# Kernel tuning notes

Hardware: AMD Instinct MI355X
Metric: run time of the kernel (lower is better)

## Reference

```python
import jax, jax.numpy as jnp
import numpy as np

N, E = 50000, 800000
DIM_IN, DIM_H, DIM_OUT, HEADS = 128, 16, 64, 8
NEG_SLOPE = 0.2  # PyG GATv2Conv default


def setup_inputs() -> dict:
    key = jax.random.key(0)
    ks = jax.random.split(key, 10)
    s = 0.1
    x = jax.random.normal(ks[0], (N, DIM_IN), jnp.float32)
    edge_index = jax.random.randint(ks[1], (2, E), 0, N, dtype=jnp.int32)
    Wl1 = jax.random.normal(ks[2], (DIM_IN, HEADS * DIM_H), jnp.float32) * s
    Wr1 = jax.random.normal(ks[3], (DIM_IN, HEADS * DIM_H), jnp.float32) * s
    att1 = jax.random.normal(ks[4], (HEADS, DIM_H), jnp.float32) * s
    b1 = jnp.zeros((HEADS * DIM_H,), jnp.float32)
    Wl2 = jax.random.normal(ks[5], (HEADS * DIM_H, DIM_OUT), jnp.float32) * s
    Wr2 = jax.random.normal(ks[6], (HEADS * DIM_H, DIM_OUT), jnp.float32) * s
    att2 = jax.random.normal(ks[7], (1, DIM_OUT), jnp.float32) * s
    b2 = jnp.zeros((DIM_OUT,), jnp.float32)
    return dict(x=x, edge_index=edge_index, Wl1=Wl1, Wr1=Wr1, att1=att1, b1=b1,
                Wl2=Wl2, Wr2=Wr2, att2=att2, b2=b2)


def gatv2_conv(x, src, dst, Wl, Wr, att, bias, heads, out_ch):
    # PyG GATv2Conv (share_weights=False, concat=True)
    n = x.shape[0]
    xl = (x @ Wl).reshape(n, heads, out_ch)  # source-side transform
    xr = (x @ Wr).reshape(n, heads, out_ch)  # target-side transform
    e = jax.nn.leaky_relu(xl[src] + xr[dst], NEG_SLOPE)          # [E, H, C]
    logits = jnp.einsum('ehc,hc->eh', e, att)                    # [E, H]
    # segment softmax over incoming edges of each dst node
    m = jax.lax.stop_gradient(jax.ops.segment_max(logits, dst, num_segments=n))
    ex = jnp.exp(logits - m[dst])
    denom = jax.ops.segment_sum(ex, dst, num_segments=n)
    alpha = ex / denom[dst]                                      # [E, H]
    out = jax.ops.segment_sum(xl[src] * alpha[..., None], dst, num_segments=n)
    return out.reshape(n, heads * out_ch) + bias


def reference(x, edge_index, Wl1, Wr1, att1, b1, Wl2, Wr2, att2, b2):
    n = x.shape[0]
    loops = jnp.arange(n, dtype=edge_index.dtype)
    src = jnp.concatenate([edge_index[0], loops])  # add_self_loops=True
    dst = jnp.concatenate([edge_index[1], loops])
    h = gatv2_conv(x, src, dst, Wl1, Wr1, att1, b1, HEADS, DIM_H)
    h = jax.nn.elu(h)
    out = gatv2_conv(h, src, dst, Wl2, Wr2, att2, b2, 1, DIM_OUT)
    return jax.nn.log_softmax(out, axis=1)
```

## Files before the change

kernel.cpp:

```cpp
#include <hip/hip_runtime.h>
#include <cstdint>

#define DIM_IN 128
#define HEADS 8
#define DIM_H 16
#define H1 128
#define DIM_OUT 64
#define NEG 0.2f
#define CAP 6144
#define P1CH 1024

typedef __attribute__((ext_vector_type(8))) short bf16x8;
typedef __attribute__((ext_vector_type(4))) float f32x4;

__device__ __forceinline__ float blo(uint32_t u) { return __uint_as_float(u << 16); }
__device__ __forceinline__ float bhi(uint32_t u) { return __uint_as_float(u & 0xffff0000u); }
__device__ __forceinline__ unsigned short f2b(float f) {
  uint32_t u = __float_as_uint(f);
  u += 0x7fffu + ((u >> 16) & 1u);
  return (unsigned short)(u >> 16);
}

#define KP 0.86561702453337804f
#define KM 0.57707801635558536f

__global__ __launch_bounds__(256) void prep_p1_fused(
    const float* __restrict__ x, unsigned short* __restrict__ xb, int totx,
    const float* __restrict__ W0, const float* __restrict__ W1,
    const float* __restrict__ W2, const float* __restrict__ W3,
    unsigned short* __restrict__ T0, unsigned short* __restrict__ T1,
    unsigned short* __restrict__ T2, unsigned short* __restrict__ T3,
    int xblocks, int p1b,
    const int* __restrict__ ei, int* __restrict__ gcnt,
    uint32_t* __restrict__ gbuf, int E, int nbkt) {
  __shared__ int sh[768];
  int bx = blockIdx.x;
  if (bx < p1b) {
    int* hist = sh;
    int* base = sh + 256;
    int* cur  = sh + 512;
    int tid = threadIdx.x;
    hist[tid] = 0;
    __syncthreads();
    int e0 = bx * P1CH;
    int nE = min(P1CH, E - e0);
    for (int i = tid; i < nE; i += 256)
      atomicAdd(&hist[ei[E + e0 + i] >> 8], 1);
    __syncthreads();
    if (tid < nbkt) {
      int h = hist[tid];
      base[tid] = h ? atomicAdd(&gcnt[tid], h) : 0;
    }
    cur[tid] = 0;
    __syncthreads();
    for (int i = tid; i < nE; i += 256) {
      int d = ei[E + e0 + i];
      int s = ei[e0 + i];
      int b = d >> 8;
      int r = atomicAdd(&cur[b], 1);
      int pos = base[b] + r;
      if (pos < CAP) gbuf[(size_t)b * CAP + pos] = ((uint32_t)d << 16) | (uint32_t)s;
    }
  } else if (bx < p1b + xblocks) {
    int i = ((bx - p1b) * 256 + threadIdx.x) * 8;
    if (i >= totx) return;
    float4 a = *(const float4*)(x + i);
    float4 b = *(const float4*)(x + i + 4);
    ushort4 u0 = {f2b(a.x), f2b(a.y), f2b(a.z), f2b(a.w)};
    ushort4 u1 = {f2b(b.x), f2b(b.y), f2b(b.z), f2b(b.w)};
    *(ushort4*)(xb + i) = u0;
    *(ushort4*)(xb + i + 4) = u1;
  } else {
    int wz = bx - p1b - xblocks;
    int z = wz >> 6;
    const float* W = (z == 0) ? W0 : (z == 1) ? W1 : (z == 2) ? W2 : W3;
    unsigned short* T = (z == 0) ? T0 : (z == 1) ? T1 : (z == 2) ? T2 : T3;
    int M = (z < 2) ? 128 : 64;
    int t = (wz & 63) * 256 + threadIdx.x;
    if (t >= M * 128) return;
    int n = t >> 7, k = t & 127;
    T[t] = f2b(W[k * M + n]);
  }
}

__device__ __forceinline__ int block_excl_scan256(int v, int* tmp) {
  int lane = threadIdx.x & 63, wid = threadIdx.x >> 6;
  int x = v;
#pragma unroll
  for (int o = 1; o < 64; o <<= 1) {
    int y = __shfl_up(x, o, 64);
    if (lane >= o) x += y;
  }
  if (lane == 63) tmp[wid] = x;
  __syncthreads();
  int prefix = 0;
#pragma unroll
  for (int w = 0; w < 4; ++w) if (w < wid) prefix += tmp[w];
  __syncthreads();
  return prefix + x - v;
}

template <int M>
__global__ __launch_bounds__(256) void gemm_mfma(
    const unsigned short* __restrict__ A,
    const unsigned short* __restrict__ Bt0, const unsigned short* __restrict__ Bt1,
    unsigned short* __restrict__ C0, unsigned short* __restrict__ C1, int Nrows,
    int gbx,
    const uint32_t* __restrict__ gbuf, const int* __restrict__ gcnt,
    int* __restrict__ off, int* __restrict__ srcs, int Np, int nbkt) {
  constexpr int K = 128;
  constexpr int LDA = 72;
  constexpr int MT = M / 2;
  constexpr int NT = MT / 16;
  __shared__ __align__(16) short Asm[128 * LDA];
  __shared__ __align__(16) short Bsm[M * LDA];
  if (blockIdx.x >= gbx) {
    if (blockIdx.z != 0) return;
    int* sb   = (int*)Asm;
    int* hist = sb + 256;
    int* cur  = hist + 256;
    int* tmp  = cur + 256;
    int b = blockIdx.x - gbx, tid = threadIdx.x;
    int gv = (tid < nbkt) ? gcnt[tid] : 0;
    int gex = block_excl_scan256(gv, tmp);
    sb[tid] = gex;
    hist[tid] = 0;
    __syncthreads();
    int base = sb[b];
    int cnt = min(gcnt[b], CAP);
    const uint32_t* p = gbuf + (size_t)b * CAP;
    for (int i = tid; i < cnt; i += 256)
      atomicAdd(&hist[(p[i] >> 16) & 255], 1);
    __syncthreads();
    int d = hist[tid];
    int excl = block_excl_scan256(d, tmp);
    int idx = (b << 8) + tid;
    int o = base + excl;
    if (idx <= Np) off[idx] = o;
    cur[tid] = o;
    __syncthreads();
    for (int i = tid; i < cnt; i += 256) {
      uint32_t v = p[i];
      int pos = atomicAdd(&cur[(v >> 16) & 255], 1);
      srcs[pos] = (int)(v & 0xFFFFu);
    }
    return;
  }
  const unsigned short* __restrict__ Bt = blockIdx.z ? Bt1 : Bt0;
  unsigned short* __restrict__ Cb = blockIdx.z ? C1 : C0;
  const int row0 = blockIdx.x * 128;
  const int tid = threadIdx.x;
  const int w = tid >> 6, lane = tid & 63;
  const int l = lane & 15, q = lane >> 4;
  const int wrow = (w >> 1) * 64, wcol = (w & 1) * MT;

  f32x4 zero = {0.f, 0.f, 0.f, 0.f};
  f32x4 acc[4][NT];
#pragma unroll
  for (int ti = 0; ti < 4; ++ti)
#pragma unroll
    for (int tj = 0; tj < NT; ++tj) acc[ti][tj] = zero;

  for (int k0 = 0; k0 < K; k0 += 64) {
    __syncthreads();
    {
      int r = tid >> 1, sg = (tid & 1) * 32;
      int grow = row0 + r;
      const uint4* src = (const uint4*)(A + (size_t)grow * K + k0 + sg);
      uint4 z4 = make_uint4(0, 0, 0, 0);
#pragma unroll
      for (int i = 0; i < 4; ++i) {
        uint4 v = (grow < Nrows) ? src[i] : z4;
        *(uint4*)(Asm + r * LDA + sg + i * 8) = v;
      }
    }
    {
      int r = tid >> 1, sg = (tid & 1) * 32;
      if (r < M) {
        const uint4* src = (const uint4*)(Bt + (size_t)r * K + k0 + sg);
#pragma unroll
        for (int i = 0; i < 4; ++i)
          *(uint4*)(Bsm + r * LDA + sg + i * 8) = src[i];
      }
    }
    __syncthreads();
#pragma unroll
    for (int kk = 0; kk < 64; kk += 32) {
      bf16x8 af[4], bfr[NT];
#pragma unroll
      for (int ti = 0; ti < 4; ++ti)
        af[ti] = *(const bf16x8*)(Asm + (wrow + ti * 16 + l) * LDA + kk + q * 8);
#pragma unroll
      for (int tj = 0; tj < NT; ++tj)
        bfr[tj] = *(const bf16x8*)(Bsm + (wcol + tj * 16 + l) * LDA + kk + q * 8);
#pragma unroll
      for (int ti = 0; ti < 4; ++ti)
#pragma unroll
        for (int tj = 0; tj < NT; ++tj)
          acc[ti][tj] = __builtin_amdgcn_mfma_f32_16x16x32_bf16(
              af[ti], bfr[tj], acc[ti][tj], 0, 0, 0);
    }
  }
#pragma unroll
  for (int ti = 0; ti < 4; ++ti) {
#pragma unroll
    for (int tj = 0; tj < NT; ++tj) {
      int col = wcol + tj * 16 + l;
#pragma unroll
      for (int r = 0; r < 4; ++r) {
        int grow = row0 + wrow + ti * 16 + q * 4 + r;
        if (grow < Nrows) Cb[(size_t)grow * M + col] = f2b(acc[ti][tj][r]);
      }
    }
  }
}

__global__ __launch_bounds__(256) void agg_l1(
    const int* __restrict__ srcs, const int* __restrict__ off,
    const unsigned short* __restrict__ xlb, const unsigned short* __restrict__ xrb,
    const float* __restrict__ att, const float* __restrict__ b1,
    unsigned short* __restrict__ hbb, int N) {
  int wid = threadIdx.x >> 6, lane = threadIdx.x & 63;
  int node = blockIdx.x * 4 + wid;
  if (node >= N) return;
  const int l4 = lane & 15;
  const int g  = lane >> 4;
  uint4 xru = *(const uint4*)(xrb + ((size_t)node << 7) + (l4 << 3));
  float r0 = blo(xru.x), r1 = bhi(xru.x), r2 = blo(xru.y), r3 = bhi(xru.y);
  float r4 = blo(xru.z), r5 = bhi(xru.z), r6 = blo(xru.w), r7 = bhi(xru.w);
  float4 a0  = *(const float4*)(att + (l4 << 3));
  float4 a1  = *(const float4*)(att + (l4 << 3) + 4);
  float c0 = KP * a0.x, c1 = KP * a0.y, c2 = KP * a0.z, c3 = KP * a0.w;
  float c4 = KP * a1.x, c5 = KP * a1.y, c6 = KP * a1.z, c7 = KP * a1.w;
  float d0 = KM * a0.x, d1 = KM * a0.y, d2 = KM * a0.z, d3 = KM * a0.w;
  float d4 = KM * a1.x, d5 = KM * a1.y, d6 = KM * a1.z, d7 = KM * a1.w;
  float acc0 = 0.f, acc1 = 0.f, acc2 = 0.f, acc3 = 0.f;
  float acc4 = 0.f, acc5 = 0.f, acc6 = 0.f, acc7 = 0.f;
  float dsum = 0.f;
  int beg = off[node];
  int M = off[node + 1] - beg + 1;
  for (int base = 0; base < M; base += 64) {
    int nk = min(64, M - base);
    int v = base + lane;
    int sv = 0;
    if (lane < nk) sv = (v == 0) ? node : srcs[beg + v - 1];
    int niter = (nk + 3) >> 2;
    for (int it = 0; it < niter; ++it) {
      int j = (it << 2) + g;
      int s = __shfl(sv, j, 64);
      uint4 xu = *(const uint4*)(xlb + ((size_t)s << 7) + (l4 << 3));
      float x0 = blo(xu.x), x1 = bhi(xu.x), x2 = blo(xu.y), x3 = bhi(xu.y);
      float x4 = blo(xu.z), x5 = bhi(xu.z), x6 = blo(xu.w), x7 = bhi(xu.w);
      float t, p;
      t = x0 + r0; p = fmaf(d0, fabsf(t), c0 * t);
      t = x1 + r1; p = fmaf(c1, t, p); p = fmaf(d1, fabsf(t), p);
      t = x2 + r2; p = fmaf(c2, t, p); p = fmaf(d2, fabsf(t), p);
      t = x3 + r3; p = fmaf(c3, t, p); p = fmaf(d3, fabsf(t), p);
      t = x4 + r4; p = fmaf(c4, t, p); p = fmaf(d4, fabsf(t), p);
      t = x5 + r5; p = fmaf(c5, t, p); p = fmaf(d5, fabsf(t), p);
      t = x6 + r6; p = fmaf(c6, t, p); p = fmaf(d6, fabsf(t), p);
      t = x7 + r7; p = fmaf(c7, t, p); p = fmaf(d7, fabsf(t), p);
      p += __shfl_xor(p, 1, 64);
      float ev = (j < nk) ? __builtin_amdgcn_exp2f(p) : 0.f;
      acc0 = fmaf(ev, x0, acc0); acc1 = fmaf(ev, x1, acc1);
      acc2 = fmaf(ev, x2, acc2); acc3 = fmaf(ev, x3, acc3);
      acc4 = fmaf(ev, x4, acc4); acc5 = fmaf(ev, x5, acc5);
      acc6 = fmaf(ev, x6, acc6); acc7 = fmaf(ev, x7, acc7);
      dsum += ev;
    }
  }
#pragma unroll
  for (int o = 16; o <= 32; o <<= 1) {
    dsum += __shfl_xor(dsum, o, 64);
    acc0 += __shfl_xor(acc0, o, 64); acc1 += __shfl_xor(acc1, o, 64);
    acc2 += __shfl_xor(acc2, o, 64); acc3 += __shfl_xor(acc3, o, 64);
    acc4 += __shfl_xor(acc4, o, 64); acc5 += __shfl_xor(acc5, o, 64);
    acc6 += __shfl_xor(acc6, o, 64); acc7 += __shfl_xor(acc7, o, 64);
  }
  if (g == 0) {
    float inv = 1.0f / dsum;
    float4 bv0 = *(const float4*)(b1 + (l4 << 3));
    float4 bv1 = *(const float4*)(b1 + (l4 << 3) + 4);
    float o0 = fmaf(acc0, inv, bv0.x), o1 = fmaf(acc1, inv, bv0.y);
    float o2 = fmaf(acc2, inv, bv0.z), o3 = fmaf(acc3, inv, bv0.w);
    float o4 = fmaf(acc4, inv, bv1.x), o5 = fmaf(acc5, inv, bv1.y);
    float o6 = fmaf(acc6, inv, bv1.z), o7 = fmaf(acc7, inv, bv1.w);
    o0 = o0 > 0.f ? o0 : expm1f(o0); o1 = o1 > 0.f ? o1 : expm1f(o1);
    o2 = o2 > 0.f ? o2 : expm1f(o2); o3 = o3 > 0.f ? o3 : expm1f(o3);
    o4 = o4 > 0.f ? o4 : expm1f(o4); o5 = o5 > 0.f ? o5 : expm1f(o5);
    o6 = o6 > 0.f ? o6 : expm1f(o6); o7 = o7 > 0.f ? o7 : expm1f(o7);
    ushort4 h0 = {f2b(o0), f2b(o1), f2b(o2), f2b(o3)};
    ushort4 h1 = {f2b(o4), f2b(o5), f2b(o6), f2b(o7)};
    unsigned short* ph = hbb + ((size_t)node << 7) + (l4 << 3);
    *(ushort4*)(ph)     = h0;
    *(ushort4*)(ph + 4) = h1;
  }
}

__global__ __launch_bounds__(256) void agg_l2(
    const int* __restrict__ srcs, const int* __restrict__ off,
    const unsigned short* __restrict__ xlb, const unsigned short* __restrict__ xrb,
    const float* __restrict__ att, const float* __restrict__ b2,
    float* __restrict__ out, int N) {
  int wid = threadIdx.x >> 6, lane = threadIdx.x & 63;
  int node = blockIdx.x * 4 + wid;
  if (node >= N) return;
  const int l3 = lane & 7;
  const int g  = lane >> 3;
  uint4 xru = *(const uint4*)(xrb + ((size_t)node << 6) + (l3 << 3));
  float r0 = blo(xru.x), r1 = bhi(xru.x), r2 = blo(xru.y), r3 = bhi(xru.y);
  float r4 = blo(xru.z), r5 = bhi(xru.z), r6 = blo(xru.w), r7 = bhi(xru.w);
  float4 a0  = *(const float4*)(att + (l3 << 3));
  float4 a1  = *(const float4*)(att + (l3 << 3) + 4);
  float c0 = KP * a0.x, c1 = KP * a0.y, c2 = KP * a0.z, c3 = KP * a0.w;
  float c4 = KP * a1.x, c5 = KP * a1.y, c6 = KP * a1.z, c7 = KP * a1.w;
  float d0 = KM * a0.x, d1 = KM * a0.y, d2 = KM * a0.z, d3 = KM * a0.w;
  float d4 = KM * a1.x, d5 = KM * a1.y, d6 = KM * a1.z, d7 = KM * a1.w;
  float acc0 = 0.f, acc1 = 0.f, acc2 = 0.f, acc3 = 0.f;
  float acc4 = 0.f, acc5 = 0.f, acc6 = 0.f, acc7 = 0.f;
  float dsum = 0.f;
  int beg = off[node];
  int M = off[node + 1] - beg + 1;
  for (int base = 0; base < M; base += 64) {
    int nk = min(64, M - base);
    int v = base + lane;
    int sv = 0;
    if (lane < nk) sv = (v == 0) ? node : srcs[beg + v - 1];
    int niter = (nk + 7) >> 3;
    for (int it = 0; it < niter; ++it) {
      int j = (it << 3) + g;
      int s = __shfl(sv, j, 64);
      uint4 xu = *(const uint4*)(xlb + ((size_t)s << 6) + (l3 << 3));
      float x0 = blo(xu.x), x1 = bhi(xu.x), x2 = blo(xu.y), x3 = bhi(xu.y);
      float x4 = blo(xu.z), x5 = bhi(xu.z), x6 = blo(xu.w), x7 = bhi(xu.w);
      float t, p;
      t = x0 + r0; p = fmaf(d0, fabsf(t), c0 * t);
      t = x1 + r1; p = fmaf(c1, t, p); p = fmaf(d1, fabsf(t), p);
      t = x2 + r2; p = fmaf(c2, t, p); p = fmaf(d2, fabsf(t), p);
      t = x3 + r3; p = fmaf(c3, t, p); p = fmaf(d3, fabsf(t), p);
      t = x4 + r4; p = fmaf(c4, t, p); p = fmaf(d4, fabsf(t), p);
      t = x5 + r5; p = fmaf(c5, t, p); p = fmaf(d5, fabsf(t), p);
      t = x6 + r6; p = fmaf(c6, t, p); p = fmaf(d6, fabsf(t), p);
      t = x7 + r7; p = fmaf(c7, t, p); p = fmaf(d7, fabsf(t), p);
      p += __shfl_xor(p, 1, 64);
      p += __shfl_xor(p, 2, 64);
      p += __shfl_xor(p, 4, 64);
      float ev = (j < nk) ? __builtin_amdgcn_exp2f(p) : 0.f;
      acc0 = fmaf(ev, x0, acc0); acc1 = fmaf(ev, x1, acc1);
      acc2 = fmaf(ev, x2, acc2); acc3 = fmaf(ev, x3, acc3);
      acc4 = fmaf(ev, x4, acc4); acc5 = fmaf(ev, x5, acc5);
      acc6 = fmaf(ev, x6, acc6); acc7 = fmaf(ev, x7, acc7);
      dsum += ev;
    }
  }
#pragma unroll
  for (int o = 8; o <= 32; o <<= 1) {
    dsum += __shfl_xor(dsum, o, 64);
    acc0 += __shfl_xor(acc0, o, 64); acc1 += __shfl_xor(acc1, o, 64);
    acc2 += __shfl_xor(acc2, o, 64); acc3 += __shfl_xor(acc3, o, 64);
    acc4 += __shfl_xor(acc4, o, 64); acc5 += __shfl_xor(acc5, o, 64);
    acc6 += __shfl_xor(acc6, o, 64); acc7 += __shfl_xor(acc7, o, 64);
  }
  float inv = 1.0f / dsum;
  float4 bv0 = *(const float4*)(b2 + (l3 << 3));
  float4 bv1 = *(const float4*)(b2 + (l3 << 3) + 4);
  float v0 = fmaf(acc0, inv, bv0.x), v1 = fmaf(acc1, inv, bv0.y);
  float v2 = fmaf(acc2, inv, bv0.z), v3 = fmaf(acc3, inv, bv0.w);
  float v4 = fmaf(acc4, inv, bv1.x), v5 = fmaf(acc5, inv, bv1.y);
  float v6 = fmaf(acc6, inv, bv1.z), v7 = fmaf(acc7, inv, bv1.w);
  float m = fmaxf(fmaxf(fmaxf(v0, v1), fmaxf(v2, v3)),
                  fmaxf(fmaxf(v4, v5), fmaxf(v6, v7)));
#pragma unroll
  for (int o = 1; o <= 4; o <<= 1) m = fmaxf(m, __shfl_xor(m, o, 64));
  float s = __expf(v0 - m) + __expf(v1 - m) + __expf(v2 - m) + __expf(v3 - m)
          + __expf(v4 - m) + __expf(v5 - m) + __expf(v6 - m) + __expf(v7 - m);
#pragma unroll
  for (int o = 1; o <= 4; o <<= 1) s += __shfl_xor(s, o, 64);
  if (g == 0) {
    float ls = __logf(s) + m;
    float* po = out + ((size_t)node << 6) + (l3 << 3);
    *(float4*)(po)     = make_float4(v0 - ls, v1 - ls, v2 - ls, v3 - ls);
    *(float4*)(po + 4) = make_float4(v4 - ls, v5 - ls, v6 - ls, v7 - ls);
  }
}

extern "C" void kernel_launch(void* const* d_in, const int* in_sizes, int n_in,
                              void* d_out, int out_size, void* d_ws, size_t ws_size,
                              hipStream_t stream) {
  const float* x    = (const float*)d_in[0];
  const int*   ei   = (const int*)d_in[1];
  const float* Wl1  = (const float*)d_in[2];
  const float* Wr1  = (const float*)d_in[3];
  const float* att1 = (const float*)d_in[4];
  const float* b1   = (const float*)d_in[5];
  const float* Wl2  = (const float*)d_in[6];
  const float* Wr2  = (const float*)d_in[7];
  const float* att2 = (const float*)d_in[8];
  const float* b2   = (const float*)d_in[9];
  float* out = (float*)d_out;

  const int N = in_sizes[0] / DIM_IN;
  const int E = in_sizes[1] / 2;
  const int nb = (N + 255) / 256;

  unsigned short* us = (unsigned short*)d_ws;
  const size_t szNH = (size_t)N * H1;
  unsigned short* xb   = us;
  unsigned short* xlb1 = xb + szNH;
  unsigned short* xrb1 = xlb1 + szNH;
  unsigned short* hbb  = xrb1 + szNH;
  unsigned short* xlb2 = hbb + szNH;
  unsigned short* xrb2 = xlb2 + (size_t)N * DIM_OUT;
  unsigned short* wt0  = xrb2 + (size_t)N * DIM_OUT;
  unsigned short* wt1  = wt0 + 16384;
  unsigned short* wt2  = wt1 + 16384;
  unsigned short* wt3  = wt2 + 8192;
  int* ibase  = (int*)(wt3 + 8192);
  int* off    = ibase;
  int* gcnt   = ibase + N + 1;
  int* srcs   = ibase + N + 1 + 256;
  uint32_t* gbuf = (uint32_t*)(srcs + E);

  const int totx = N * DIM_IN;
  const int xblocks = (totx / 8 + 255) / 256;
  const int p1b = (E + P1CH - 1) / P1CH;
  const int gb = (N + 127) / 128;

  hipMemsetAsync(gcnt, 0, 256 * sizeof(int), stream);

  prep_p1_fused<<<p1b + xblocks + 256, 256, 0, stream>>>(
      x, xb, totx, Wl1, Wr1, Wl2, Wr2, wt0, wt1, wt2, wt3, xblocks, p1b,
      ei, gcnt, gbuf, E, nb);

  gemm_mfma<128><<<dim3(gb + nb, 1, 2), 256, 0, stream>>>(
      xb, wt0, wt1, xlb1, xrb1, N, gb, gbuf, gcnt, off, srcs, N, nb);

  agg_l1<<<(N + 3) / 4, 256, 0, stream>>>(srcs, off, xlb1, xrb1, att1, b1, hbb, N);

  gemm_mfma<64><<<dim3(gb, 1, 2), 256, 0, stream>>>(
      hbb, wt2, wt3, xlb2, xrb2, N, gb, nullptr, nullptr, nullptr, nullptr, N, nb);

  agg_l2<<<(N + 3) / 4, 256, 0, stream>>>(srcs, off, xlb2, xrb2, att2, b2, out, N);
}
```

Baseline: 233.8 us.

## Precompute per-source linear attention term via folded W·att projections

Uses the identity leaky_relu(t) = KP·t + KM·|t| (up to scaling) to split the attention logit into a linear part and an absolute-value part. The linear part is precomputed per source node as x·(W·att), folded from the weights in the prep kernel and computed in spare gemm blocks. The per-edge inner loop then drops eight multiply-adds and gathers one extra float per edge. The cost is new small kernels' worth of work in the gemm launches and an extra gather stream. Numerics shift slightly because the linear term now comes from unrounded fp32 weights rather than the bf16 products.

```diff
diff --git a/kernel.cpp b/kernel.cpp
--- a/kernel.cpp
+++ b/kernel.cpp
@@ -32,7 +32,9 @@
     unsigned short* __restrict__ T2, unsigned short* __restrict__ T3,
     int xblocks, int p1b,
     const int* __restrict__ ei, int* __restrict__ gcnt,
-    uint32_t* __restrict__ gbuf, int E, int nbkt) {
+    uint32_t* __restrict__ gbuf, int E, int nbkt,
+    const float* __restrict__ att1, const float* __restrict__ att2,
+    float* __restrict__ v1f, float* __restrict__ v2f) {
   __shared__ int sh[768];
   int bx = blockIdx.x;
   if (bx < p1b) {
@@ -70,7 +72,7 @@
     ushort4 u1 = {f2b(b.x), f2b(b.y), f2b(b.z), f2b(b.w)};
     *(ushort4*)(xb + i) = u0;
     *(ushort4*)(xb + i + 4) = u1;
-  } else {
+  } else if (bx < p1b + xblocks + 256) {
     int wz = bx - p1b - xblocks;
     int z = wz >> 6;
     const float* W = (z == 0) ? W0 : (z == 1) ? W1 : (z == 2) ? W2 : W3;
@@ -80,6 +82,28 @@
     if (t >= M * 128) return;
     int n = t >> 7, k = t & 127;
     T[t] = f2b(W[k * M + n]);
+  } else {
+    int vb = bx - p1b - xblocks - 256;
+    int t = threadIdx.x;
+    if (vb == 0) {
+      int k = t >> 1, hb = (t & 1) * 4;
+#pragma unroll
+      for (int h2 = 0; h2 < 4; ++h2) {
+        int h = hb + h2;
+        float s = 0.f;
+#pragma unroll
+        for (int c = 0; c < 16; ++c)
+          s = fmaf(W0[k * 128 + h * 16 + c], att1[h * 16 + c], s);
+        v1f[h * 128 + k] = 0.5f * KP * s;
+      }
+    } else {
+      if (t < 128) {
+        float s = 0.f;
+        for (int c = 0; c < 64; ++c)
+          s = fmaf(W2[t * 64 + c], att2[c], s);
+        v2f[t] = (KP / 8.0f) * s;
+      }
+    }
   }
 }
 
@@ -107,42 +131,92 @@
     unsigned short* __restrict__ C0, unsigned short* __restrict__ C1, int Nrows,
     int gbx,
     const uint32_t* __restrict__ gbuf, const int* __restrict__ gcnt,
-    int* __restrict__ off, int* __restrict__ srcs, int Np, int nbkt) {
+    int* __restrict__ off, int* __restrict__ srcs, int Np, int nbkt,
+    const unsigned short* __restrict__ usrc, const float* __restrict__ vf,
+    float* __restrict__ uout, int ublocks) {
   constexpr int K = 128;
   constexpr int LDA = 72;
   constexpr int MT = M / 2;
   constexpr int NT = MT / 16;
+  constexpr int NH = (M == 128) ? 8 : 1;
   __shared__ __align__(16) short Asm[128 * LDA];
   __shared__ __align__(16) short Bsm[M * LDA];
   if (blockIdx.x >= gbx) {
-    if (blockIdx.z != 0) return;
-    int* sb   = (int*)Asm;
-    int* hist = sb + 256;
-    int* cur  = hist + 256;
-    int* tmp  = cur + 256;
-    int b = blockIdx.x - gbx, tid = threadIdx.x;
-    int gv = (tid < nbkt) ? gcnt[tid] : 0;
-    int gex = block_excl_scan256(gv, tmp);
-    sb[tid] = gex;
-    hist[tid] = 0;
-    __syncthreads();
-    int base = sb[b];
-    int cnt = min(gcnt[b], CAP);
-    const uint32_t* p = gbuf + (size_t)b * CAP;
-    for (int i = tid; i < cnt; i += 256)
-      atomicAdd(&hist[(p[i] >> 16) & 255], 1);
-    __syncthreads();
-    int d = hist[tid];
-    int excl = block_excl_scan256(d, tmp);
-    int idx = (b << 8) + tid;
-    int o = base + excl;
-    if (idx <= Np) off[idx] = o;
-    cur[tid] = o;
-    __syncthreads();
-    for (int i = tid; i < cnt; i += 256) {
-      uint32_t v = p[i];
-      int pos = atomicAdd(&cur[(v >> 16) & 255], 1);
-      srcs[pos] = (int)(v & 0xFFFFu);
+    int ab = blockIdx.x - gbx;
+    if (blockIdx.z == 0) {
+      if (ab >= nbkt) return;
+      int* sb   = (int*)Asm;
+      int* hist = sb + 256;
+      int* cur  = hist + 256;
+      int* tmp  = cur + 256;
+      int b = ab, tid = threadIdx.x;
+      int gv = (tid < nbkt) ? gcnt[tid] : 0;
+      int gex = block_excl_scan256(gv, tmp);
+      sb[tid] = gex;
+      hist[tid] = 0;
+      __syncthreads();
+      int base = sb[b];
+      int cnt = min(gcnt[b], CAP);
+      const uint32_t* p = gbuf + (size_t)b * CAP;
+      for (int i = tid; i < cnt; i += 256)
+        atomicAdd(&hist[(p[i] >> 16) & 255], 1);
+      __syncthreads();
+      int d = hist[tid];
+      int excl = block_excl_scan256(d, tmp);
+      int idx = (b << 8) + tid;
+      int o = base + excl;
+      if (idx <= Np) off[idx] = o;
+      cur[tid] = o;
+      __syncthreads();
+      for (int i = tid; i < cnt; i += 256) {
+        uint32_t v = p[i];
+        int pos = atomicAdd(&cur[(v >> 16) & 255], 1);
+        srcs[pos] = (int)(v & 0xFFFFu);
+      }
+    } else {
+      if (ab >= ublocks) return;
+      float* vl = (float*)Asm;
+      int tid = threadIdx.x;
+      for (int i2 = tid; i2 < 128 * NH; i2 += 256) vl[i2] = vf[i2];
+      __syncthreads();
+      int i = tid & 15, nn = tid >> 4;
+#pragma unroll
+      for (int r = 0; r < 4; ++r) {
+        int n = ab * 64 + r * 16 + nn;
+        float ps[NH];
+#pragma unroll
+        for (int h = 0; h < NH; ++h) ps[h] = 0.f;
+        if (n < Np) {
+          uint4 xu = *(const uint4*)(usrc + ((size_t)n << 7) + (i << 3));
+          float m0 = blo(xu.x), m1 = bhi(xu.x), m2 = blo(xu.y), m3 = bhi(xu.y);
+          float m4 = blo(xu.z), m5 = bhi(xu.z), m6 = blo(xu.w), m7 = bhi(xu.w);
+#pragma unroll
+          for (int h = 0; h < NH; ++h) {
+            const float* vk = vl + h * 128 + i * 8;
+            float4 va = *(const float4*)(vk);
+            float4 vb2 = *(const float4*)(vk + 4);
+            float s = m0 * va.x;
+            s = fmaf(m1, va.y, s); s = fmaf(m2, va.z, s); s = fmaf(m3, va.w, s);
+            s = fmaf(m4, vb2.x, s); s = fmaf(m5, vb2.y, s);
+            s = fmaf(m6, vb2.z, s); s = fmaf(m7, vb2.w, s);
+            ps[h] = s;
+          }
+        }
+#pragma unroll
+        for (int o = 1; o < 16; o <<= 1)
+#pragma unroll
+          for (int h = 0; h < NH; ++h) ps[h] += __shfl_xor(ps[h], o, 64);
+        if (i == 0 && n < Np) {
+          if (NH == 8) {
+            float4 w0 = {ps[0], ps[1], ps[2], ps[3]};
+            float4 w1 = {ps[4], ps[5], ps[6], ps[7]};
+            *(float4*)(uout + ((size_t)n << 3))     = w0;
+            *(float4*)(uout + ((size_t)n << 3) + 4) = w1;
+          } else {
+            uout[n] = ps[0];
+          }
+        }
+      }
     }
     return;
   }
@@ -219,7 +293,7 @@
     const int* __restrict__ srcs, const int* __restrict__ off,
     const unsigned short* __restrict__ xlb, const unsigned short* __restrict__ xrb,
     const float* __restrict__ att, const float* __restrict__ b1,
-    unsigned short* __restrict__ hbb, int N) {
+    const float* __restrict__ u1, unsigned short* __restrict__ hbb, int N) {
   int wid = threadIdx.x >> 6, lane = threadIdx.x & 63;
   int node = blockIdx.x * 4 + wid;
   if (node >= N) return;
@@ -230,13 +304,12 @@
   float r4 = blo(xru.z), r5 = bhi(xru.z), r6 = blo(xru.w), r7 = bhi(xru.w);
   float4 a0  = *(const float4*)(att + (l4 << 3));
   float4 a1  = *(const float4*)(att + (l4 << 3) + 4);
-  float c0 = KP * a0.x, c1 = KP * a0.y, c2 = KP * a0.z, c3 = KP * a0.w;
-  float c4 = KP * a1.x, c5 = KP * a1.y, c6 = KP * a1.z, c7 = KP * a1.w;
   float d0 = KM * a0.x, d1 = KM * a0.y, d2 = KM * a0.z, d3 = KM * a0.w;
   float d4 = KM * a1.x, d5 = KM * a1.y, d6 = KM * a1.z, d7 = KM * a1.w;
   float acc0 = 0.f, acc1 = 0.f, acc2 = 0.f, acc3 = 0.f;
   float acc4 = 0.f, acc5 = 0.f, acc6 = 0.f, acc7 = 0.f;
   float dsum = 0.f;
+  const uint32_t loU = (uint32_t)((l4 >> 1) << 2);
   int beg = off[node];
   int M = off[node + 1] - beg + 1;
   for (int base = 0; base < M; base += 64) {
@@ -248,18 +321,19 @@
     for (int it = 0; it < niter; ++it) {
       int j = (it << 2) + g;
       int s = __shfl(sv, j, 64);
+      float up = *(const float*)((const char*)u1 + ((((uint32_t)s) << 5) | loU));
       uint4 xu = *(const uint4*)(xlb + ((size_t)s << 7) + (l4 << 3));
       float x0 = blo(xu.x), x1 = bhi(xu.x), x2 = blo(xu.y), x3 = bhi(xu.y);
       float x4 = blo(xu.z), x5 = bhi(xu.z), x6 = blo(xu.w), x7 = bhi(xu.w);
       float t, p;
-      t = x0 + r0; p = fmaf(d0, fabsf(t), c0 * t);
-      t = x1 + r1; p = fmaf(c1, t, p); p = fmaf(d1, fabsf(t), p);
-      t = x2 + r2; p = fmaf(c2, t, p); p = fmaf(d2, fabsf(t), p);
-      t = x3 + r3; p = fmaf(c3, t, p); p = fmaf(d3, fabsf(t), p);
-      t = x4 + r4; p = fmaf(c4, t, p); p = fmaf(d4, fabsf(t), p);
-      t = x5 + r5; p = fmaf(c5, t, p); p = fmaf(d5, fabsf(t), p);
-      t = x6 + r6; p = fmaf(c6, t, p); p = fmaf(d6, fabsf(t), p);
-      t = x7 + r7; p = fmaf(c7, t, p); p = fmaf(d7, fabsf(t), p);
+      t = x0 + r0; p = fmaf(d0, fabsf(t), up);
+      t = x1 + r1; p = fmaf(d1, fabsf(t), p);
+      t = x2 + r2; p = fmaf(d2, fabsf(t), p);
+      t = x3 + r3; p = fmaf(d3, fabsf(t), p);
+      t = x4 + r4; p = fmaf(d4, fabsf(t), p);
+      t = x5 + r5; p = fmaf(d5, fabsf(t), p);
+      t = x6 + r6; p = fmaf(d6, fabsf(t), p);
+      t = x7 + r7; p = fmaf(d7, fabsf(t), p);
       p += __shfl_xor(p, 1, 64);
       float ev = (j < nk) ? __builtin_amdgcn_exp2f(p) : 0.f;
       acc0 = fmaf(ev, x0, acc0); acc1 = fmaf(ev, x1, acc1);
@@ -301,7 +375,7 @@
     const int* __restrict__ srcs, const int* __restrict__ off,
     const unsigned short* __restrict__ xlb, const unsigned short* __restrict__ xrb,
     const float* __restrict__ att, const float* __restrict__ b2,
-    float* __restrict__ out, int N) {
+    const float* __restrict__ u2, float* __restrict__ out, int N) {
   int wid = threadIdx.x >> 6, lane = threadIdx.x & 63;
   int node = blockIdx.x * 4 + wid;
   if (node >= N) return;
@@ -312,8 +386,6 @@
   float r4 = blo(xru.z), r5 = bhi(xru.z), r6 = blo(xru.w), r7 = bhi(xru.w);
   float4 a0  = *(const float4*)(att + (l3 << 3));
   float4 a1  = *(const float4*)(att + (l3 << 3) + 4);
-  float c0 = KP * a0.x, c1 = KP * a0.y, c2 = KP * a0.z, c3 = KP * a0.w;
-  float c4 = KP * a1.x, c5 = KP * a1.y, c6 = KP * a1.z, c7 = KP * a1.w;
   float d0 = KM * a0.x, d1 = KM * a0.y, d2 = KM * a0.z, d3 = KM * a0.w;
   float d4 = KM * a1.x, d5 = KM * a1.y, d6 = KM * a1.z, d7 = KM * a1.w;
   float acc0 = 0.f, acc1 = 0.f, acc2 = 0.f, acc3 = 0.f;
@@ -330,18 +402,19 @@
     for (int it = 0; it < niter; ++it) {
       int j = (it << 3) + g;
       int s = __shfl(sv, j, 64);
+      float up = u2[s];
       uint4 xu = *(const uint4*)(xlb + ((size_t)s << 6) + (l3 << 3));
       float x0 = blo(xu.x), x1 = bhi(xu.x), x2 = blo(xu.y), x3 = bhi(xu.y);
       float x4 = blo(xu.z), x5 = bhi(xu.z), x6 = blo(xu.w), x7 = bhi(xu.w);
       float t, p;
-      t = x0 + r0; p = fmaf(d0, fabsf(t), c0 * t);
-      t = x1 + r1; p = fmaf(c1, t, p); p = fmaf(d1, fabsf(t), p);
-      t = x2 + r2; p = fmaf(c2, t, p); p = fmaf(d2, fabsf(t), p);
-      t = x3 + r3; p = fmaf(c3, t, p); p = fmaf(d3, fabsf(t), p);
-      t = x4 + r4; p = fmaf(c4, t, p); p = fmaf(d4, fabsf(t), p);
-      t = x5 + r5; p = fmaf(c5, t, p); p = fmaf(d5, fabsf(t), p);
-      t = x6 + r6; p = fmaf(c6, t, p); p = fmaf(d6, fabsf(t), p);
-      t = x7 + r7; p = fmaf(c7, t, p); p = fmaf(d7, fabsf(t), p);
+      t = x0 + r0; p = fmaf(d0, fabsf(t), up);
+      t = x1 + r1; p = fmaf(d1, fabsf(t), p);
+      t = x2 + r2; p = fmaf(d2, fabsf(t), p);
+      t = x3 + r3; p = fmaf(d3, fabsf(t), p);
+      t = x4 + r4; p = fmaf(d4, fabsf(t), p);
+      t = x5 + r5; p = fmaf(d5, fabsf(t), p);
+      t = x6 + r6; p = fmaf(d6, fabsf(t), p);
+      t = x7 + r7; p = fmaf(d7, fabsf(t), p);
       p += __shfl_xor(p, 1, 64);
       p += __shfl_xor(p, 2, 64);
       p += __shfl_xor(p, 4, 64);
@@ -420,25 +493,34 @@
   int* gcnt   = ibase + N + 1;
   int* srcs   = ibase + N + 1 + 256;
   uint32_t* gbuf = (uint32_t*)(srcs + E);
+  float* v1f = (float*)(gbuf + (size_t)nb * CAP);
+  float* v2f = v1f + 1024;
+  float* u1s = v2f + 128;
+  float* u2s = u1s + (size_t)N * 8;
 
   const int totx = N * DIM_IN;
   const int xblocks = (totx / 8 + 255) / 256;
   const int p1b = (E + P1CH - 1) / P1CH;
   const int gb = (N + 127) / 128;
+  const int ub = (N + 63) / 64;
 
   hipMemsetAsync(gcnt, 0, 256 * sizeof(int), stream);
 
-  prep_p1_fused<<<p1b + xblocks + 256, 256, 0, stream>>>(
+  prep_p1_fused<<<p1b + xblocks + 256 + 2, 256, 0, stream>>>(
       x, xb, totx, Wl1, Wr1, Wl2, Wr2, wt0, wt1, wt2, wt3, xblocks, p1b,
-      ei, gcnt, gbuf, E, nb);
-
-  gemm_mfma<128><<<dim3(gb + nb, 1, 2), 256, 0, stream>>>(
-      xb, wt0, wt1, xlb1, xrb1, N, gb, gbuf, gcnt, off, srcs, N, nb);
-
-  agg_l1<<<(N + 3) / 4, 256, 0, stream>>>(srcs, off, xlb1, xrb1, att1, b1, hbb, N);
-
-  gemm_mfma<64><<<dim3(gb, 1, 2), 256, 0, stream>>>(
-      hbb, wt2, wt3, xlb2, xrb2, N, gb, nullptr, nullptr, nullptr, nullptr, N, nb);
-
-  agg_l2<<<(N + 3) / 4, 256, 0, stream>>>(srcs, off, xlb2, xrb2, att2, b2, out, N);
-}
+      ei, gcnt, gbuf, E, nb, att1, att2, v1f, v2f);
+
+  gemm_mfma<128><<<dim3(gb + ((ub > nb) ? ub : nb), 1, 2), 256, 0, stream>>>(
+      xb, wt0, wt1, xlb1, xrb1, N, gb, gbuf, gcnt, off, srcs, N, nb,
+      xb, v1f, u1s, ub);
+
+  agg_l1<<<(N + 3) / 4, 256, 0, stream>>>(srcs, off, xlb1, xrb1, att1, b1,
+                                          u1s, hbb, N);
+
+  gemm_mfma<64><<<dim3(gb + ub, 1, 2), 256, 0, stream>>>(
+      hbb, wt2, wt3, xlb2, xrb2, N, gb, gbuf, gcnt, off, srcs, N, 0,
+      hbb, v2f, u2s, ub);
+
+  agg_l2<<<(N + 3) / 4, 256, 0, stream>>>(srcs, off, xlb2, xrb2, att2, b2,
+                                          u2s, out, N);
+}
```

New measurement: 237.5 us. About the same (+1.6%).
